# Kernel tuning notes

Measured on AMD Instinct MI355X. Metric: run time of the kernel, lower is better.

## Reference

```python
import jax, jax.numpy as jnp
import numpy as np

EPS = 1e-5

def setup_inputs() -> dict:
    key = jax.random.key(0)
    k1, k2, k3 = jax.random.split(key, 3)
    x = jax.random.normal(k1, (16, 256, 32, 32), dtype=jnp.float32)
    embed = jax.random.normal(k2, (8192, 256), dtype=jnp.float32)
    cluster_size = jax.random.uniform(k3, (8192,), dtype=jnp.float32)
    return {"x": x, "embed": embed, "cluster_size": cluster_size}

def reference(x, embed, cluster_size):
    # x: (b, c, h, w) -> (b, h*w, c); project_in is Identity (codebook_dim == dim, heads=1)
    b, c, h, w = x.shape
    xt = jnp.transpose(x, (0, 2, 3, 1)).reshape(b, h * w, c)   # (b, n, d)
    flat = xt.reshape(-1, c)                                    # (N, d)
    d2 = (jnp.sum(flat * flat, axis=1, keepdims=True)
          - 2.0 * flat @ embed.T
          + jnp.sum(embed * embed, axis=1))                     # (N, K)
    embed_ind_flat = jnp.argmin(d2, axis=-1)                    # (N,) temperature==0 -> argmax of -d2
    quantize = embed[embed_ind_flat].reshape(b, h * w, c)       # gather codebook rows
    embed_ind = embed_ind_flat.reshape(b, h * w)
    # perplexity over (unnormalized) EMA cluster sizes, as in the torch code
    probs = cluster_size
    perplexity = jnp.exp(-jnp.sum(probs * jnp.log(probs + EPS)))
    # eval-mode commitment loss (weight_loss=True, commitment_weight=1.0)
    commit_loss = jnp.mean((quantize - xt) ** 2)
    return quantize, embed_ind, perplexity, commit_loss
```

## Files before the change

### kernel.cpp

```cpp
#include <hip/hip_runtime.h>
#include <hip/hip_bf16.h>
#include <math.h>

typedef _Float16 f16x8 __attribute__((ext_vector_type(8)));
typedef float f32x4 __attribute__((ext_vector_type(4)));

#define N_TOK 16384
#define D 256
#define K 8192

#define Q_OFF 0
#define IND_OFF 4194304
#define PERP_OFF 4210688
#define COMMIT_OFF 4210689

#define WS_CAND   0u
#define WS_E2     1048576u
#define WS_DSUM   1081344u
#define WS_EH     1114112u
#define WS_XH     5308416u
#define WS_XT     13697024u
#define WS_NEED   30474240u

__device__ __forceinline__ unsigned int ford(float f) {
    unsigned int u = __float_as_uint(f);
    return (u & 0x80000000u) ? ~u : (u | 0x80000000u);
}
__device__ __forceinline__ unsigned short f2h(float f) {
    _Float16 h = (_Float16)f;
    return *(unsigned short*)&h;
}
__device__ __forceinline__ void gload16(const void* g, void* l) {
    __builtin_amdgcn_global_load_lds(
        (const __attribute__((address_space(1))) unsigned int*)g,
        (__attribute__((address_space(3))) unsigned int*)l, 16, 0, 0);
}


__global__ void vq_convert_x(const float* __restrict__ x, float* __restrict__ xt,
                             unsigned short* __restrict__ xh) {
    __shared__ float t[64][65];
    const int tid = threadIdx.x;
    const int p0 = blockIdx.x * 64, c0 = blockIdx.y * 64, b = blockIdx.z;
    const int q = tid & 15, h = tid >> 4;
    #pragma unroll
    for (int r = 0; r < 4; ++r) {
        const int cl = r * 16 + h;
        const float4 v = *(const float4*)(x + (((size_t)(b * 256 + c0 + cl)) << 10) + p0 + q * 4);
        t[cl][q * 4 + 0] = v.x; t[cl][q * 4 + 1] = v.y;
        t[cl][q * 4 + 2] = v.z; t[cl][q * 4 + 3] = v.w;
    }
    __syncthreads();
    #pragma unroll
    for (int r = 0; r < 4; ++r) {
        const int nl = r * 16 + h;
        const int n = (b << 10) + p0 + nl;
        const int c = c0 + q * 4;
        float4 vf; ushort4 vh;
        vf.x = t[q * 4 + 0][nl]; vf.y = t[q * 4 + 1][nl];
        vf.z = t[q * 4 + 2][nl]; vf.w = t[q * 4 + 3][nl];
        vh.x = f2h(vf.x); vh.y = f2h(vf.y); vh.z = f2h(vf.z); vh.w = f2h(vf.w);
        *(float4*)(xt + ((size_t)n << 8) + c) = vf;
        *(ushort4*)(xh + ((size_t)n << 8) + c) = vh;
    }
}

__global__ void vq_prep_e(const float* __restrict__ e, unsigned short* __restrict__ eh,
                          float* __restrict__ e2, double* __restrict__ dsum) {
    if (blockIdx.x == 0 && threadIdx.x == 0) *dsum = 0.0;
    const int wave = threadIdx.x >> 6, lane = threadIdx.x & 63;
    const int c = blockIdx.x * 4 + wave;
    const float4 v = *(const float4*)(e + (size_t)c * D + lane * 4);
    ushort4 vh;
    vh.x = f2h(v.x); vh.y = f2h(v.y); vh.z = f2h(v.z); vh.w = f2h(v.w);
    *(ushort4*)(eh + (size_t)c * D + lane * 4) = vh;
    float s = v.x * v.x + v.y * v.y + v.z * v.z + v.w * v.w;
    #pragma unroll
    for (int off = 32; off > 0; off >>= 1) s += __shfl_down(s, off, 64);
    if (lane == 0) e2[c] = s;
}

__global__ __launch_bounds__(256)
__attribute__((amdgpu_waves_per_eu(2, 2)))
void vq_mfma_kernel(
    const unsigned short* __restrict__ xh, const unsigned short* __restrict__ eh,
    const float* __restrict__ e2, unsigned int* __restrict__ cand) {
    __shared__ __align__(16) unsigned short Bs[4][3][2048];
    __shared__ float e2s[1024];

    const int tid = threadIdx.x;
    const int lane = tid & 63, wid = tid >> 6;
    const int l15 = lane & 15, lg = lane >> 4;
    const int split = blockIdx.y;
    const int m0 = blockIdx.x * 256;
    const int c0s = split * 1024;
    const int rw = m0 + wid * 64;
    char* wb = (char*)&Bs[wid][0][0];

    *(float4*)&e2s[tid * 4] = *(const float4*)(e2 + c0s + tid * 4);
    __syncthreads();

    f16x8 a[4][8];
    #pragma unroll
    for (int mf = 0; mf < 4; ++mf) {
        const unsigned short* ap = xh + (((size_t)(rw + mf * 16 + l15)) << 8) + lg * 8;
        #pragma unroll
        for (int t = 0; t < 8; ++t)
            a[mf][t] = *(const f16x8*)(ap + t * 32);
    }
    #pragma unroll
    for (int mf = 0; mf < 4; ++mf)
        #pragma unroll
        for (int t = 0; t < 8; ++t)
            asm volatile("" : "+v"(*(f32x4*)&a[mf][t]));

    const unsigned short* ebase =
        eh + (((size_t)c0s) << 8) + (((size_t)(lane >> 3)) << 8) +
        ((((lane & 7) ^ ((lane >> 3) & 7))) << 3);

    auto stage = [&](int s, int bo) {
        const int toff = ((s >> 2) << 13) + ((s & 3) << 6);
        const unsigned short* p = ebase + toff;
        #pragma unroll
        for (int i = 0; i < 4; ++i)
            gload16(p + (i << 11), wb + bo + i * 1024);
    };

    int boff[2][2];
    #pragma unroll
    for (int nf = 0; nf < 2; ++nf)
        #pragma unroll
        for (int ks2 = 0; ks2 < 2; ++ks2) {
            const int rb = nf * 16 + l15;
            boff[nf][ks2] = rb * 128 + (((ks2 * 4 + lg) ^ (rb & 7)) << 4);
        }

    float d1[16], d2[16];
    unsigned int ipk[16];
    #pragma unroll
    for (int r = 0; r < 16; ++r) { d1[r] = INFINITY; d2[r] = INFINITY; ipk[r] = 0; }

    int bo0 = 0, bo1 = 4096, bo2 = 8192;
    stage(0, bo0);
    stage(1, bo1);

    #pragma unroll 1
    for (int ct = 0; ct < 32; ++ct) {
        const float e2v0 = e2s[ct * 32 + l15];
        const float e2v1 = e2s[ct * 32 + 16 + l15];
        f32x4 acc[4][2];
        #pragma unroll
        for (int mf = 0; mf < 4; ++mf) {
            f32x4 z = {0.f, 0.f, 0.f, 0.f};
            acc[mf][0] = z; acc[mf][1] = z;
        }
        #pragma unroll
        for (int ks = 0; ks < 4; ++ks) {
            const int s = ct * 4 + ks;
            if (s < 126) stage(s + 2, bo2);
            if (s < 126)      asm volatile("s_waitcnt vmcnt(8)" ::: "memory");
            else if (s == 126) asm volatile("s_waitcnt vmcnt(4)" ::: "memory");
            else               asm volatile("s_waitcnt vmcnt(0)" ::: "memory");
            __builtin_amdgcn_s_setprio(1);
            #pragma unroll
            for (int ks2 = 0; ks2 < 2; ++ks2) {
                const f16x8 b0 = *(const f16x8*)(wb + bo0 + boff[0][ks2]);
                const f16x8 b1 = *(const f16x8*)(wb + bo0 + boff[1][ks2]);
                #pragma unroll
                for (int mf = 0; mf < 4; ++mf) {
                    acc[mf][0] = __builtin_amdgcn_mfma_f32_16x16x32_f16(
                        a[mf][ks * 2 + ks2], b0, acc[mf][0], 0, 0, 0);
                    acc[mf][1] = __builtin_amdgcn_mfma_f32_16x16x32_f16(
                        a[mf][ks * 2 + ks2], b1, acc[mf][1], 0, 0, 0);
                }
            }
            __builtin_amdgcn_s_setprio(0);
            const int tmp = bo0; bo0 = bo1; bo1 = bo2; bo2 = tmp;
        }
        const unsigned int cl0 = (unsigned int)(ct * 32 + l15);
        #pragma unroll
        for (int mf = 0; mf < 4; ++mf) {
            #pragma unroll
            for (int reg = 0; reg < 4; ++reg) {
                const int rr = mf * 4 + reg;
                const float sc0 = fmaf(-2.0f, acc[mf][0][reg], e2v0);
                const float sc1 = fmaf(-2.0f, acc[mf][1][reg], e2v1);
                if (fminf(sc0, sc1) < d2[rr]) {
                    {
                        const bool lt1 = sc0 < d1[rr], lt2 = sc0 < d2[rr];
                        const unsigned int ii = ipk[rr];
                        const unsigned int nif = (ii << 16) | cl0;
                        const unsigned int nis = (ii & 0xFFFFu) | (cl0 << 16);
                        d2[rr] = lt1 ? d1[rr] : (lt2 ? sc0 : d2[rr]);
                        ipk[rr] = lt1 ? nif : (lt2 ? nis : ii);
                        d1[rr] = lt1 ? sc0 : d1[rr];
                    }
                    {
                        const unsigned int cl1 = cl0 + 16;
                        const bool lt1 = sc1 < d1[rr], lt2 = sc1 < d2[rr];
                        const unsigned int ii = ipk[rr];
                        const unsigned int nif = (ii << 16) | cl1;
                        const unsigned int nis = (ii & 0xFFFFu) | (cl1 << 16);
                        d2[rr] = lt1 ? d1[rr] : (lt2 ? sc1 : d2[rr]);
                        ipk[rr] = lt1 ? nif : (lt2 ? nis : ii);
                        d1[rr] = lt1 ? sc1 : d1[rr];
                    }
                }
            }
        }
    }

    unsigned long long p1[16], p2[16];
    #pragma unroll
    for (int r = 0; r < 16; ++r) {
        p1[r] = (((unsigned long long)ford(d1[r])) << 32) |
                (unsigned int)(c0s + (ipk[r] & 0xFFFFu));
        p2[r] = (((unsigned long long)ford(d2[r])) << 32) |
                (unsigned int)(c0s + (ipk[r] >> 16));
    }
    #pragma unroll
    for (int st = 1; st < 16; st <<= 1) {
        #pragma unroll
        for (int r = 0; r < 16; ++r) {
            const unsigned long long q1 = __shfl_xor(p1[r], st, 64);
            const unsigned long long q2 = __shfl_xor(p2[r], st, 64);
            const unsigned long long n1 = p1[r] < q1 ? p1[r] : q1;
            const unsigned long long hi = p1[r] < q1 ? q1 : p1[r];
            const unsigned long long l2 = p2[r] < q2 ? p2[r] : q2;
            p1[r] = n1;
            p2[r] = hi < l2 ? hi : l2;
        }
    }
    if (l15 == 0) {
        #pragma unroll
        for (int mf = 0; mf < 4; ++mf)
            #pragma unroll
            for (int reg = 0; reg < 4; ++reg) {
                const int n = rw + mf * 16 + lg * 4 + reg;
                unsigned int* cp = cand + (((size_t)n) << 4) + split * 2;
                cp[0] = (unsigned int)p1[mf * 4 + reg];
                cp[1] = (unsigned int)p2[mf * 4 + reg];
            }
    }
}

__global__ void vq_rescore_finalize(const float* __restrict__ xt, const float* __restrict__ embed,
                                    const float* __restrict__ e2,
                                    const unsigned int* __restrict__ cand,
                                    float* __restrict__ out, double* __restrict__ dsum) {
    __shared__ double red[4];
    const int tid = threadIdx.x, wid = tid >> 6, lane = tid & 63;
    double wsum = 0.0;
    #pragma unroll 1
    for (int it = 0; it < 8; ++it) {
        const int n = blockIdx.x * 32 + it * 4 + wid;
        const float4 xv = *(const float4*)(xt + (((size_t)n) << 8) + lane * 4);
        unsigned long long best = 0xFFFFFFFFFFFFFFFFull;
        #pragma unroll 2
        for (int j = 0; j < 16; ++j) {
            const unsigned int c = cand[(((size_t)n) << 4) + j];
            const float4 ev = *(const float4*)(embed + (((size_t)c) << 8) + lane * 4);
            float dt = xv.x * ev.x + xv.y * ev.y + xv.z * ev.z + xv.w * ev.w;
            #pragma unroll
            for (int off = 32; off > 0; off >>= 1) dt += __shfl_xor(dt, off, 64);
            const float s = fmaf(-2.0f, dt, e2[c]);
            const unsigned long long p = (((unsigned long long)ford(s)) << 32) | c;
            best = p < best ? p : best;
        }
        const unsigned int bi = (unsigned int)(best & 0xFFFFFFFFull);
        if (lane == 0) out[IND_OFF + n] = (float)bi;
        const float4 ev = *(const float4*)(embed + (((size_t)bi) << 8) + lane * 4);
        *(float4*)(out + Q_OFF + (((size_t)n) << 8) + lane * 4) = ev;
        const float q0 = ev.x - xv.x, q1 = ev.y - xv.y, q2 = ev.z - xv.z, q3 = ev.w - xv.w;
        float a4 = q0 * q0 + q1 * q1 + q2 * q2 + q3 * q3;
        #pragma unroll
        for (int off = 32; off > 0; off >>= 1) a4 += __shfl_xor(a4, off, 64);
        if (lane == 0) wsum += (double)a4;
    }
    if (lane == 0) red[wid] = wsum;
    __syncthreads();
    if (tid == 0) atomicAdd(dsum, red[0] + red[1] + red[2] + red[3]);
}

__global__ void vq_tail_kernel(const float* __restrict__ cs,
                               const double* __restrict__ dsum,
                               float* __restrict__ out) {
    __shared__ double red[4];
    const int tid = threadIdx.x;
    double s = 0.0;
    for (int i = tid; i < K; i += 256) {
        const float p = cs[i];
        s += (double)(p * logf(p + 1e-5f));
    }
    #pragma unroll
    for (int off = 32; off > 0; off >>= 1) s += __shfl_down(s, off, 64);
    if ((tid & 63) == 0) red[tid >> 6] = s;
    __syncthreads();
    if (tid == 0) {
        const double tot = red[0] + red[1] + red[2] + red[3];
        const double pv = exp(-tot);
        out[PERP_OFF] = (pv > 3.3e38) ? 3.3e38f : (float)pv;
        out[COMMIT_OFF] = (float)(*dsum * (1.0 / 4194304.0));
    }
}

#define TM 64
#define TN 64
#define BKF 32
#define NSPLITF 2
#define CODES_PER_SPLIT (K / NSPLITF)
#define TILES_PER_SPLIT (CODES_PER_SPLIT / TN)

__global__ void vq_init_kernel(unsigned long long* __restrict__ keys, double* __restrict__ dsum) {
    int i = blockIdx.x * blockDim.x + threadIdx.x;
    if (i < N_TOK) keys[i] = 0xFFFFFFFFFFFFFFFFull;
    if (i == 0) *dsum = 0.0;
}
__global__ void vq_e2_kernel(const float* __restrict__ embed, float* __restrict__ e2) {
    int wave = threadIdx.x >> 6, lane = threadIdx.x & 63;
    int c = blockIdx.x * 4 + wave;
    const float4 v = *(const float4*)(embed + (size_t)c * D + lane * 4);
    float s = v.x * v.x + v.y * v.y + v.z * v.z + v.w * v.w;
    #pragma unroll
    for (int off = 32; off > 0; off >>= 1) s += __shfl_down(s, off, 64);
    if (lane == 0) e2[c] = s;
}
__global__ __launch_bounds__(256, 2) void vq_argmin_kernel(
    const float* __restrict__ x, const float* __restrict__ embed,
    const float* __restrict__ e2, unsigned long long* __restrict__ keys) {
    __shared__ float xT[D][TM];
    __shared__ float eT[BKF][TN + 4];
    const int tid = threadIdx.x;
    const int n0 = blockIdx.x * TM;
    const int b = n0 >> 10, p0 = n0 & 1023;
    const float* xb = x + (size_t)b * D * 1024 + p0;
    {
        const int t4 = (tid & 15) * 4, chb = tid >> 4;
        #pragma unroll
        for (int pass = 0; pass < 16; ++pass) {
            const int ch = pass * 16 + chb;
            *(float4*)&xT[ch][t4] = *(const float4*)(xb + (size_t)ch * 1024 + t4);
        }
    }
    __syncthreads();
    const int tm4 = (tid & 15) * 4, tn = tid >> 4, tn4 = tn * 4;
    float bestd[4]; int besti[4];
    #pragma unroll
    for (int i = 0; i < 4; ++i) { bestd[i] = INFINITY; besti[i] = 0x7fffffff; }
    for (int ct = 0; ct < TILES_PER_SPLIT; ++ct) {
        const int c0 = blockIdx.y * CODES_PER_SPLIT + ct * TN;
        float acc[4][4] = {};
        for (int kk = 0; kk < D; kk += BKF) {
            {
                const int j = tid >> 2, ch4 = (tid & 3) * 4;
                #pragma unroll
                for (int p = 0; p < 2; ++p) {
                    const int chl = p * 16 + ch4;
                    const float4 ev = *(const float4*)(embed + (size_t)(c0 + j) * D + kk + chl);
                    eT[chl + 0][j] = ev.x; eT[chl + 1][j] = ev.y;
                    eT[chl + 2][j] = ev.z; eT[chl + 3][j] = ev.w;
                }
            }
            __syncthreads();
            #pragma unroll
            for (int k2 = 0; k2 < BKF; ++k2) {
                const float4 a = *(const float4*)&xT[kk + k2][tm4];
                const float4 bv = *(const float4*)&eT[k2][tn4];
                acc[0][0] += a.x * bv.x; acc[0][1] += a.x * bv.y; acc[0][2] += a.x * bv.z; acc[0][3] += a.x * bv.w;
                acc[1][0] += a.y * bv.x; acc[1][1] += a.y * bv.y; acc[1][2] += a.y * bv.z; acc[1][3] += a.y * bv.w;
                acc[2][0] += a.z * bv.x; acc[2][1] += a.z * bv.y; acc[2][2] += a.z * bv.z; acc[2][3] += a.z * bv.w;
                acc[3][0] += a.w * bv.x; acc[3][1] += a.w * bv.y; acc[3][2] += a.w * bv.z; acc[3][3] += a.w * bv.w;
            }
            __syncthreads();
        }
        #pragma unroll
        for (int j = 0; j < 4; ++j) {
            const int c = c0 + tn4 + j;
            const float ec = e2[c];
            #pragma unroll
            for (int i = 0; i < 4; ++i) {
                const float s = ec - 2.0f * acc[i][j];
                if (s < bestd[i]) { bestd[i] = s; besti[i] = c; }
            }
        }
    }
    __syncthreads();
    float* cd = &eT[0][0];
    int* ci = (int*)&eT[16][0];
    #pragma unroll
    for (int i = 0; i < 4; ++i) { cd[tn * 64 + tm4 + i] = bestd[i]; ci[tn * 64 + tm4 + i] = besti[i]; }
    __syncthreads();
    if (tid < TM) {
        float bd = INFINITY; int bi = 0x7fffffff;
        for (int j = 0; j < 16; ++j) {
            const float d = cd[j * 64 + tid]; const int idx = ci[j * 64 + tid];
            if (d < bd || (d == bd && idx < bi)) { bd = d; bi = idx; }
        }
        atomicMin(&keys[n0 + tid], (((unsigned long long)ford(bd)) << 32) | (unsigned int)bi);
    }
}
__global__ void vq_finalize_kernel(const float* __restrict__ x, const float* __restrict__ embed,
                                   const unsigned long long* __restrict__ keys,
                                   float* __restrict__ out, double* __restrict__ dsum) {
    const int tid = threadIdx.x;
    const int n0 = blockIdx.x * 64;
    const int t = tid >> 2, q = tid & 3;
    const int n = n0 + t;
    const int b = n >> 10, p = n & 1023;
    if (tid < 64) {
        const int nn = n0 + tid;
        out[IND_OFF + nn] = (float)(int)(unsigned int)(keys[nn] & 0xFFFFFFFFull);
    }
    const int idx = (int)(unsigned int)(keys[n] & 0xFFFFFFFFull);
    const float* erow = embed + (size_t)idx * D;
    const float* xrow = x + (size_t)b * D * 1024 + p;
    float* qrow = out + Q_OFF + (size_t)n * D;
    float acc = 0.0f;
    #pragma unroll
    for (int i = 0; i < 16; ++i) {
        const int ch = i * 16 + q * 4;
        const float4 ev = *(const float4*)(erow + ch);
        *(float4*)(qrow + ch) = ev;
        const float x0 = xrow[(size_t)(ch + 0) * 1024];
        const float x1 = xrow[(size_t)(ch + 1) * 1024];
        const float x2 = xrow[(size_t)(ch + 2) * 1024];
        const float x3 = xrow[(size_t)(ch + 3) * 1024];
        const float d0 = ev.x - x0, d1 = ev.y - x1, d2 = ev.z - x2, d3 = ev.w - x3;
        acc += d0 * d0 + d1 * d1 + d2 * d2 + d3 * d3;
    }
    #pragma unroll
    for (int off = 32; off > 0; off >>= 1) acc += __shfl_down(acc, off, 64);
    if ((tid & 63) == 0) atomicAdd(dsum, (double)acc);
}

extern "C" void kernel_launch(void* const* d_in, const int* in_sizes, int n_in,
                              void* d_out, int out_size, void* d_ws, size_t ws_size,
                              hipStream_t stream) {
    const float* x = (const float*)d_in[0];
    const float* embed = (const float*)d_in[1];
    const float* cs = (const float*)d_in[2];
    float* out = (float*)d_out;
    char* ws = (char*)d_ws;

    if (ws_size >= (size_t)WS_NEED) {
        unsigned int* cand = (unsigned int*)(ws + WS_CAND);
        float* e2 = (float*)(ws + WS_E2);
        double* dsum = (double*)(ws + WS_DSUM);
        unsigned short* eh = (unsigned short*)(ws + WS_EH);
        unsigned short* xh = (unsigned short*)(ws + WS_XH);
        float* xt = (float*)(ws + WS_XT);

        vq_prep_e<<<dim3(K / 4), dim3(256), 0, stream>>>(embed, eh, e2, dsum);
        vq_convert_x<<<dim3(16, 4, 16), dim3(256), 0, stream>>>(x, xt, xh);
        vq_mfma_kernel<<<dim3(64, 8), dim3(256), 0, stream>>>(xh, eh, e2, cand);
        vq_rescore_finalize<<<dim3(512), dim3(256), 0, stream>>>(xt, embed, e2, cand, out, dsum);
        vq_tail_kernel<<<dim3(1), dim3(256), 0, stream>>>(cs, dsum, out);
    } else {
        unsigned long long* keys = (unsigned long long*)ws;
        float* e2 = (float*)(ws + 131072);
        double* dsum = (double*)(ws + 163840);
        vq_init_kernel<<<dim3(64), dim3(256), 0, stream>>>(keys, dsum);
        vq_e2_kernel<<<dim3(K / 4), dim3(256), 0, stream>>>(embed, e2);
        vq_argmin_kernel<<<dim3(N_TOK / TM, NSPLITF), dim3(256), 0, stream>>>(x, embed, e2, keys);
        vq_finalize_kernel<<<dim3(256), dim3(256), 0, stream>>>(x, embed, keys, out, dsum);
        vq_tail_kernel<<<dim3(1), dim3(256), 0, stream>>>(cs, dsum, out);
    }
}
```

Measured before the change: 196.4 us.

## Share codebook tiles across waves via block-wide LDS staging with barriers

Each of the four waves previously streamed the full codebook slice into its own private LDS buffers, so every block fetched the same data four times. Now all 256 threads load one shared 32-code by 256-dim tile per step into a triple-buffered LDS ring, with a swizzled layout and a block barrier each iteration. This cuts global and L2 traffic for the codebook by four. In exchange it adds a barrier per tile, which couples the waves and can stall MFMA issue.

```diff
diff --git a/kernel.cpp b/kernel.cpp
--- a/kernel.cpp
+++ b/kernel.cpp
@@ -85,7 +85,7 @@
 void vq_mfma_kernel(
     const unsigned short* __restrict__ xh, const unsigned short* __restrict__ eh,
     const float* __restrict__ e2, unsigned int* __restrict__ cand) {
-    __shared__ __align__(16) unsigned short Bs[4][3][2048];
+    __shared__ __align__(16) unsigned short Bs[3][32 * 256];
     __shared__ float e2s[1024];
 
     const int tid = threadIdx.x;
@@ -95,10 +95,8 @@
     const int m0 = blockIdx.x * 256;
     const int c0s = split * 1024;
     const int rw = m0 + wid * 64;
-    char* wb = (char*)&Bs[wid][0][0];
 
     *(float4*)&e2s[tid * 4] = *(const float4*)(e2 + c0s + tid * 4);
-    __syncthreads();
 
     f16x8 a[4][8];
     #pragma unroll
@@ -114,58 +112,58 @@
         for (int t = 0; t < 8; ++t)
             asm volatile("" : "+v"(*(f32x4*)&a[mf][t]));
 
+    __syncthreads();
+
+    const int r0 = tid >> 5, cc = tid & 31;
     const unsigned short* ebase =
-        eh + (((size_t)c0s) << 8) + (((size_t)(lane >> 3)) << 8) +
-        ((((lane & 7) ^ ((lane >> 3) & 7))) << 3);
-
-    auto stage = [&](int s, int bo) {
-        const int toff = ((s >> 2) << 13) + ((s & 3) << 6);
-        const unsigned short* p = ebase + toff;
+        eh + (((size_t)(c0s + r0)) << 8) + ((cc ^ (r0 & 7)) << 3);
+    char* wdst = (char*)Bs + tid * 16;
+
+    auto stage = [&](int t, int bo) {
+        const unsigned short* p = ebase + t * 8192;
         #pragma unroll
         for (int i = 0; i < 4; ++i)
-            gload16(p + (i << 11), wb + bo + i * 1024);
+            gload16(p + i * 2048, wdst + bo + i * 4096);
     };
 
-    int boff[2][2];
-    #pragma unroll
-    for (int nf = 0; nf < 2; ++nf)
-        #pragma unroll
-        for (int ks2 = 0; ks2 < 2; ++ks2) {
-            const int rb = nf * 16 + l15;
-            boff[nf][ks2] = rb * 128 + (((ks2 * 4 + lg) ^ (rb & 7)) << 4);
-        }
+    const int rb0 = l15 * 512;
+    const int rb1 = rb0 + 16 * 512;
+    const int rx = l15 & 7;
+    const char* wb = (const char*)Bs;
 
     float d1[16], d2[16];
     unsigned int ipk[16];
     #pragma unroll
     for (int r = 0; r < 16; ++r) { d1[r] = INFINITY; d2[r] = INFINITY; ipk[r] = 0; }
 
-    int bo0 = 0, bo1 = 4096, bo2 = 8192;
+    int bo0 = 0, bo1 = 16384, bo2 = 32768;
     stage(0, bo0);
     stage(1, bo1);
 
     #pragma unroll 1
-    for (int ct = 0; ct < 32; ++ct) {
-        const float e2v0 = e2s[ct * 32 + l15];
-        const float e2v1 = e2s[ct * 32 + 16 + l15];
+    for (int t = 0; t < 32; ++t) {
+        if (t < 31) asm volatile("s_waitcnt vmcnt(4)" ::: "memory");
+        else        asm volatile("s_waitcnt vmcnt(0)" ::: "memory");
+        __builtin_amdgcn_s_barrier();
+        if (t < 30) stage(t + 2, bo2);
+
+        const float e2v0 = e2s[t * 32 + l15];
+        const float e2v1 = e2s[t * 32 + 16 + l15];
         f32x4 acc[4][2];
         #pragma unroll
         for (int mf = 0; mf < 4; ++mf) {
             f32x4 z = {0.f, 0.f, 0.f, 0.f};
             acc[mf][0] = z; acc[mf][1] = z;
         }
+        __builtin_amdgcn_s_setprio(1);
         #pragma unroll
         for (int ks = 0; ks < 4; ++ks) {
-            const int s = ct * 4 + ks;
-            if (s < 126) stage(s + 2, bo2);
-            if (s < 126)      asm volatile("s_waitcnt vmcnt(8)" ::: "memory");
-            else if (s == 126) asm volatile("s_waitcnt vmcnt(4)" ::: "memory");
-            else               asm volatile("s_waitcnt vmcnt(0)" ::: "memory");
-            __builtin_amdgcn_s_setprio(1);
             #pragma unroll
             for (int ks2 = 0; ks2 < 2; ++ks2) {
-                const f16x8 b0 = *(const f16x8*)(wb + bo0 + boff[0][ks2]);
-                const f16x8 b1 = *(const f16x8*)(wb + bo0 + boff[1][ks2]);
+                const int kc = ks * 8 + ks2 * 4;
+                const int ko = ((kc + lg) ^ rx) << 4;
+                const f16x8 b0 = *(const f16x8*)(wb + bo0 + rb0 + ko);
+                const f16x8 b1 = *(const f16x8*)(wb + bo0 + rb1 + ko);
                 #pragma unroll
                 for (int mf = 0; mf < 4; ++mf) {
                     acc[mf][0] = __builtin_amdgcn_mfma_f32_16x16x32_f16(
@@ -174,10 +172,10 @@
                         a[mf][ks * 2 + ks2], b1, acc[mf][1], 0, 0, 0);
                 }
             }
-            __builtin_amdgcn_s_setprio(0);
-            const int tmp = bo0; bo0 = bo1; bo1 = bo2; bo2 = tmp;
-        }
-        const unsigned int cl0 = (unsigned int)(ct * 32 + l15);
+        }
+        __builtin_amdgcn_s_setprio(0);
+
+        const unsigned int cl0 = (unsigned int)(t * 32 + l15);
         #pragma unroll
         for (int mf = 0; mf < 4; ++mf) {
             #pragma unroll
@@ -208,6 +206,7 @@
                 }
             }
         }
+        const int tmp = bo0; bo0 = bo1; bo1 = bo2; bo2 = tmp;
     }
 
     unsigned long long p1[16], p2[16];
```

After: 173.2 us. -11.8%, faster.
